# Optimization experiments

Measured on AMD Instinct MI355X. Metric: run time of the kernel, lower is better.

The kernel has to match this reference:

```python
import jax, jax.numpy as jnp
import numpy as np

K = 5    # reassembly kernel size (kernel_size)
UP = 2   # upsample factor (up_factor)


def setup_inputs() -> dict:
    key = jax.random.key(0)
    k1, k2 = jax.random.split(key)
    B, C, H, W = 8, 256, 64, 64
    inp = jax.random.normal(k1, (B, C, H, W), dtype=jnp.float32)
    # per-pixel reassembly weights: up^2 * k^2 channels at low resolution
    km = jax.random.uniform(k2, (B, UP * UP * K * K, H, W), dtype=jnp.float32)
    return {"input": inp, "kernel_map": km}


def _carafe(x, km):
    # x:  [B, C, H, W]
    # km: [B, up^2 * k^2, H, W]
    B, C, H, W = x.shape
    pad = K // 2
    xp = jnp.pad(x, ((0, 0), (0, 0), (pad, pad), (pad, pad)))  # zero boundary
    # Extract kxk neighborhoods: fixed 25-iteration loop over kernel offsets
    # patches: [B, C, k*k, H, W]
    patches = jnp.stack(
        [xp[:, :, i:i + H, j:j + W] for i in range(K) for j in range(K)],
        axis=2,
    )
    # weights per sub-pixel output position: [B, up^2, k*k, H, W]
    w = km.reshape(B, UP * UP, K * K, H, W)
    # content-aware weighted reassembly
    out = jnp.einsum('bckhw,bukhw->buchw', patches, w)  # [B, up^2, C, H, W]
    # pixel-shuffle: sub-pixel index u = i*UP + j -> (h*UP+i, w*UP+j)
    out = out.reshape(B, UP, UP, C, H, W)
    out = out.transpose(0, 3, 4, 1, 5, 2)  # [B, C, H, UP, W, UP]
    return out.reshape(B, C, H * UP, W * UP)


def reference(input, kernel_map):
    return _carafe(input, kernel_map)
```

## Files before the change

kernel.cpp:

```cpp
#include <hip/hip_runtime.h>

namespace {
constexpr int Bn = 8, Cn = 256, Hn = 64, Wn = 64;
constexpr int Kk = 5, PAD = 2, KMC = 100, KK2 = 25;
constexpr int CSPLIT = 2;
constexpr int CPB = Cn / CSPLIT;
constexpr int NCB = CPB / 16;
constexpr int NWG = Hn * Bn * CSPLIT;
constexpr int NXCD = 8;
constexpr int CHUNK = NWG / NXCD;
constexpr int HW = Hn * Wn;
}

__global__ __launch_bounds__(256, 2) void carafe_fwd(
    const float* __restrict__ x,
    const float* __restrict__ km,
    float* __restrict__ out)
{
    const int wg   = blockIdx.x;
    const int orig = (wg & (NXCD - 1)) * CHUNK + (wg >> 3);
    const int cz   = orig & 1;
    const int h    = (orig >> 1) & (Hn - 1);
    const int b    = orig >> 7;

    const int tid = threadIdx.x;
    const int wv  = tid >> 6;
    const int w   = tid & 63;

    __shared__ __align__(16) float xs[4][2][Kk][68][4];
    __shared__ float kw[KK2][4][64];
    __shared__ float dummy[64];

    {
        float* slab = &xs[0][0][0][0][0];
        for (int i = tid; i < 4 * 2 * Kk * 68 * 4; i += 256) slab[i] = 0.0f;
    }

    {
        const float* kmb = km + ((size_t)b * KMC) * HW + h * Wn;
        for (int idx = tid; idx < KMC * 64; idx += 256) {
            const int ch = idx >> 6;
            const int ww = idx & 63;
            const int u  = ch / KK2;
            const int t  = ch - u * KK2;
            kw[t][u][ww] = kmb[(size_t)ch * HW + ww];
        }
    }

    __syncthreads();

    const float* xb = x + (size_t)b * Cn * HW;
    float* ob       = out + (size_t)b * Cn * (2 * Hn) * (2 * Wn);

    const int sl_ch = w & 3;
    const int sl_cl = w >> 2;

    auto STAGE = [&](int bi, int c0s) {
        #pragma unroll
        for (int r = 0; r < Kk; ++r) {
            const int hr  = h - PAD + r;
            const int hrc = hr < 0 ? 0 : (hr >= Hn ? Hn - 1 : hr);
            const bool valid = (hr == hrc);
            const float* srow =
                xb + (size_t)(c0s + sl_ch) * HW + hrc * Wn + sl_cl;
            #pragma unroll
            for (int q = 0; q < 4; ++q) {
                float* d = valid ? &xs[wv][bi][r][2 + 16 * q][0] : &dummy[0];
                __builtin_amdgcn_global_load_lds(
                    (const __attribute__((address_space(1))) void*)(srow + 16 * q),
                    (__attribute__((address_space(3))) void*)d, 4, 0, 0);
            }
        }
    };

    STAGE(0, cz * CPB + wv * 4);

    #pragma unroll 1
    for (int cb = 0; cb < NCB; ++cb) {
        const int c0 = cz * CPB + cb * 16 + wv * 4;

        if (cb + 1 < NCB)
            STAGE((cb + 1) & 1, c0 + 16);

        if (cb == 0)            asm volatile("s_waitcnt vmcnt(20)" ::: "memory");
        else if (cb + 1 < NCB)  asm volatile("s_waitcnt vmcnt(28)" ::: "memory");
        else                    asm volatile("s_waitcnt vmcnt(8)"  ::: "memory");

        const int bi = cb & 1;
        float acc[4][4] = {};
        #pragma unroll
        for (int kh = 0; kh < Kk; ++kh) {
            #pragma unroll
            for (int kwi = 0; kwi < Kk; ++kwi) {
                const int t = kh * Kk + kwi;
                const float4 tap = *(const float4*)(&xs[wv][bi][kh][w + kwi][0]);
                const float w0 = kw[t][0][w];
                const float w1 = kw[t][1][w];
                const float w2 = kw[t][2][w];
                const float w3 = kw[t][3][w];
                acc[0][0] += tap.x * w0; acc[0][1] += tap.x * w1;
                acc[0][2] += tap.x * w2; acc[0][3] += tap.x * w3;
                acc[1][0] += tap.y * w0; acc[1][1] += tap.y * w1;
                acc[1][2] += tap.y * w2; acc[1][3] += tap.y * w3;
                acc[2][0] += tap.z * w0; acc[2][1] += tap.z * w1;
                acc[2][2] += tap.z * w2; acc[2][3] += tap.z * w3;
                acc[3][0] += tap.w * w0; acc[3][1] += tap.w * w1;
                acc[3][2] += tap.w * w2; acc[3][3] += tap.w * w3;
            }
        }

        #pragma unroll
        for (int k = 0; k < 4; ++k) {
            #pragma unroll
            for (int i = 0; i < 2; ++i) {
                float2 o2 = make_float2(acc[k][2 * i + 0], acc[k][2 * i + 1]);
                *(float2*)(&ob[((size_t)(c0 + k) * (2 * Hn) + (2 * h + i)) *
                                   (2 * Wn) + 2 * w]) = o2;
            }
        }
    }
}

extern "C" void kernel_launch(void* const* d_in, const int* in_sizes, int n_in,
                              void* d_out, int out_size, void* d_ws, size_t ws_size,
                              hipStream_t stream)
{
    const float* x  = (const float*)d_in[0];
    const float* km = (const float*)d_in[1];
    float* out      = (float*)d_out;

    dim3 grid(NWG);
    carafe_fwd<<<grid, 256, 0, stream>>>(x, km, out);
}
```

Before: 200.2 us.

## Drop LDS double-buffering for higher occupancy and pack weights as float4

```diff
diff --git a/kernel.cpp b/kernel.cpp
--- a/kernel.cpp
+++ b/kernel.cpp
@@ -12,7 +12,7 @@
 constexpr int HW = Hn * Wn;
 }
 
-__global__ __launch_bounds__(256, 2) void carafe_fwd(
+__global__ __launch_bounds__(256, 4) void carafe_fwd(
     const float* __restrict__ x,
     const float* __restrict__ km,
     float* __restrict__ out)
@@ -27,13 +27,13 @@
     const int wv  = tid >> 6;
     const int w   = tid & 63;
 
-    __shared__ __align__(16) float xs[4][2][Kk][68][4];
-    __shared__ float kw[KK2][4][64];
+    __shared__ __align__(16) float xs[4][Kk][68][4];
+    __shared__ __align__(16) float4 kw4[KK2][64];
     __shared__ float dummy[64];
 
     {
-        float* slab = &xs[0][0][0][0][0];
-        for (int i = tid; i < 4 * 2 * Kk * 68 * 4; i += 256) slab[i] = 0.0f;
+        float* slab = &xs[wv][0][0][0];
+        for (int i = w; i < Kk * 68 * 4; i += 64) slab[i] = 0.0f;
     }
 
     {
@@ -43,7 +43,7 @@
             const int ww = idx & 63;
             const int u  = ch / KK2;
             const int t  = ch - u * KK2;
-            kw[t][u][ww] = kmb[(size_t)ch * HW + ww];
+            ((float*)&kw4[t][ww])[u] = kmb[(size_t)ch * HW + ww];
         }
     }
 
@@ -55,7 +55,7 @@
     const int sl_ch = w & 3;
     const int sl_cl = w >> 2;
 
-    auto STAGE = [&](int bi, int c0s) {
+    auto STAGE = [&](int c0s) {
         #pragma unroll
         for (int r = 0; r < Kk; ++r) {
             const int hr  = h - PAD + r;
@@ -65,7 +65,7 @@
                 xb + (size_t)(c0s + sl_ch) * HW + hrc * Wn + sl_cl;
             #pragma unroll
             for (int q = 0; q < 4; ++q) {
-                float* d = valid ? &xs[wv][bi][r][2 + 16 * q][0] : &dummy[0];
+                float* d = valid ? &xs[wv][r][2 + 16 * q][0] : &dummy[0];
                 __builtin_amdgcn_global_load_lds(
                     (const __attribute__((address_space(1))) void*)(srow + 16 * q),
                     (__attribute__((address_space(3))) void*)d, 4, 0, 0);
@@ -73,39 +73,30 @@
         }
     };
 
-    STAGE(0, cz * CPB + wv * 4);
-
     #pragma unroll 1
     for (int cb = 0; cb < NCB; ++cb) {
         const int c0 = cz * CPB + cb * 16 + wv * 4;
 
-        if (cb + 1 < NCB)
-            STAGE((cb + 1) & 1, c0 + 16);
+        asm volatile("s_waitcnt lgkmcnt(0)" ::: "memory");
+        STAGE(c0);
+        asm volatile("s_waitcnt vmcnt(0)" ::: "memory");
 
-        if (cb == 0)            asm volatile("s_waitcnt vmcnt(20)" ::: "memory");
-        else if (cb + 1 < NCB)  asm volatile("s_waitcnt vmcnt(28)" ::: "memory");
-        else                    asm volatile("s_waitcnt vmcnt(8)"  ::: "memory");
-
-        const int bi = cb & 1;
         float acc[4][4] = {};
         #pragma unroll
         for (int kh = 0; kh < Kk; ++kh) {
             #pragma unroll
             for (int kwi = 0; kwi < Kk; ++kwi) {
                 const int t = kh * Kk + kwi;
-                const float4 tap = *(const float4*)(&xs[wv][bi][kh][w + kwi][0]);
-                const float w0 = kw[t][0][w];
-                const float w1 = kw[t][1][w];
-                const float w2 = kw[t][2][w];
-                const float w3 = kw[t][3][w];
-                acc[0][0] += tap.x * w0; acc[0][1] += tap.x * w1;
-                acc[0][2] += tap.x * w2; acc[0][3] += tap.x * w3;
-                acc[1][0] += tap.y * w0; acc[1][1] += tap.y * w1;
-                acc[1][2] += tap.y * w2; acc[1][3] += tap.y * w3;
-                acc[2][0] += tap.z * w0; acc[2][1] += tap.z * w1;
-                acc[2][2] += tap.z * w2; acc[2][3] += tap.z * w3;
-                acc[3][0] += tap.w * w0; acc[3][1] += tap.w * w1;
-                acc[3][2] += tap.w * w2; acc[3][3] += tap.w * w3;
+                const float4 tap = *(const float4*)(&xs[wv][kh][w + kwi][0]);
+                const float4 wt  = kw4[t][w];
+                acc[0][0] += tap.x * wt.x; acc[0][1] += tap.x * wt.y;
+                acc[0][2] += tap.x * wt.z; acc[0][3] += tap.x * wt.w;
+                acc[1][0] += tap.y * wt.x; acc[1][1] += tap.y * wt.y;
+                acc[1][2] += tap.y * wt.z; acc[1][3] += tap.y * wt.w;
+                acc[2][0] += tap.z * wt.x; acc[2][1] += tap.z * wt.y;
+                acc[2][2] += tap.z * wt.z; acc[2][3] += tap.z * wt.w;
+                acc[3][0] += tap.w * wt.x; acc[3][1] += tap.w * wt.y;
+                acc[3][2] += tap.w * wt.z; acc[3][3] += tap.w * wt.w;
             }
         }
 
```

Result: no change. 197.4 us (-1.4%).
